# Optimization experiments

Measured on AMD Instinct MI355X. Metric: run time of the kernel, lower is better.

Reference implementation:

```python
import jax, jax.numpy as jnp
import numpy as np

GAMMA = 0.1
ENERGY = 0.5
BATCH = 64
INF = 1e10  # finite 'infinity' so exp(-INF/gamma) underflows to exactly 0


def softdtw_batch(D, gamma):
    """Batched soft-DTW over pairwise frame-distance matrices.
    D: [P, T, T] squared-Euclidean distances. Returns R(T-1,T-1): [P].
    DP is parallelized across anti-diagonals (wavefront)."""
    P, T, _ = D.shape
    iarr = jnp.arange(T)

    def body(carry, k):
        Rm2, Rm1 = carry  # diagonals k-2 and k-1, each [P, T] indexed by row i
        j = k - iarr
        valid = (j >= 0) & (j < T)
        d = D[:, iarr, jnp.clip(j, 0, T - 1)]  # [P, T]
        pad = jnp.full((P, 1), INF, D.dtype)
        r_up = jnp.concatenate([pad, Rm1[:, :-1]], axis=1)      # R(i-1, j)
        r_left = Rm1                                            # R(i, j-1)
        corner = jnp.where(k == 0, jnp.float32(0.0), jnp.float32(INF))
        r_diag = jnp.concatenate([jnp.full((P, 1), 1.0, D.dtype) * corner,
                                  Rm2[:, :-1]], axis=1)         # R(i-1, j-1)
        z = jnp.stack([r_up, r_left, r_diag], axis=0)           # [3, P, T]
        smin = -gamma * jax.nn.logsumexp(-z / gamma, axis=0)
        Rk = jnp.where(valid[None, :], d + smin, INF)
        return (Rm1, Rk), None

    init = (jnp.full((P, T), INF, D.dtype), jnp.full((P, T), INF, D.dtype))
    (_, Rlast), _ = jax.lax.scan(body, init, jnp.arange(2 * T - 1))
    return Rlast[:, T - 1]


def setup_inputs() -> dict:
    key = jax.random.key(0)
    k1, k2 = jax.random.split(key)
    xxx = jax.random.normal(k1, (BATCH, 64, 13), dtype=jnp.float32)
    yyy = jax.random.normal(k2, (BATCH, 64, 13), dtype=jnp.float32)
    return {"xxx": xxx, "yyy": yyy}


def reference(xxx, yyy):
    B = BATCH
    full = jnp.concatenate([xxx, yyy], axis=0)  # [N, T, d]
    N, T, _ = full.shape
    # pairwise squared-Euclidean frame distances: [N, N, T, T]
    sq = jnp.sum(full * full, axis=-1)                      # [N, T]
    dots = jnp.einsum('aid,bjd->abij', full, full)          # [N, N, T, T]
    D = sq[:, None, :, None] + sq[None, :, None, :] - 2.0 * dots
    R = softdtw_batch(D.reshape(N * N, T, T), GAMMA)        # [N*N]
    sim = R.reshape(N, N)
    eye = jnp.eye(N, dtype=bool)
    sim = jnp.where(eye, 0.0, sim)  # i==j pairs skipped in original (left as 0)
    sim = sim / ENERGY
    pos = jnp.diagonal(sim, offset=B)                       # [B]
    positives = jnp.concatenate([pos, pos], axis=0)         # [2B] (source uses +B offset twice)
    loss = jnp.mean(-positives + jax.nn.logsumexp(sim, axis=-1))
    return loss
```

## Files before the change

### kernel.cpp

```cpp
#include <hip/hip_runtime.h>

#define TT 64
#define DIM 13
#define NSEQ 128
#define NPAIRS 8128
#define NWAVE 4064
#define NSTEP (TT + 32 - 1)
#define INFV 1e10f
#define C_EXP 14.4269504088896f
#define C_INV 0.06931471805599453f

typedef _Float16 h2 __attribute__((ext_vector_type(2)));

__device__ __forceinline__ float fdot2(h2 a, h2 b, float c) {
    return __builtin_amdgcn_fdot2(a, b, c, false);
}
__device__ __forceinline__ h2 mkh2(float a, float b) {
    h2 p; p.x = (_Float16)a; p.y = (_Float16)b; return p;
}
__device__ __forceinline__ h2 bch2(unsigned u) { return __builtin_bit_cast(h2, u); }
__device__ __forceinline__ float shr1_inf(float x) {
    int r = __builtin_amdgcn_update_dpp(__builtin_bit_cast(int, INFV),
                                        __builtin_bit_cast(int, x),
                                        0x138, 0xf, 0xf, false);
    return __builtin_bit_cast(float, r);
}
__device__ __forceinline__ float smstep(float S, float lf, float dg, float acc) {
    float m  = fminf(fminf(S, lf), dg);
    float md = __builtin_amdgcn_fmed3f(S, lf, dg);
    float M  = fmaxf(fmaxf(S, lf), dg);
    float s  = 1.0f + __builtin_amdgcn_exp2f(m - md) + __builtin_amdgcn_exp2f(m - M);
    return fmaf(acc, C_EXP, m - __builtin_amdgcn_logf(s));
}

__global__ __launch_bounds__(256) void sdtw_pairs(const float* __restrict__ xxx,
                                                  const float* __restrict__ yyy,
                                                  float* __restrict__ simR) {
    __shared__ unsigned xl[4][7 * 2 * TT];
    const int wave = threadIdx.x >> 6;
    const int lane = threadIdx.x & 63;
    const int half = lane >> 5;
    const int sj   = lane & 31;
    const int p = 2 * (blockIdx.x * 4 + wave) + half;

    int a = (int)((255.0f - sqrtf(65025.0f - 8.0f * (float)p)) * 0.5f);
    if (a < 0) a = 0;
    if (a > 126) a = 126;
    while (a * (255 - a) / 2 > p) a--;
    while ((a + 1) * (254 - a) / 2 <= p) a++;
    const int b = a + 1 + (p - a * (255 - a) / 2);

    h2 yA[7], yB[7];
    float sqyA = 0.f, sqyB = 0.f;
    {
        const float* fb = ((b < 64) ? xxx + (size_t)b * TT * DIM
                                    : yyy + (size_t)(b - 64) * TT * DIM) + (2 * sj) * DIM;
        float vA[DIM], vB[DIM];
#pragma unroll
        for (int c = 0; c < DIM; c++) {
            vA[c] = fb[c];        sqyA += vA[c] * vA[c];
            vB[c] = fb[DIM + c];  sqyB += vB[c] * vB[c];
        }
#pragma unroll
        for (int c = 0; c < 6; c++) {
            yA[c] = mkh2(vA[2 * c], vA[2 * c + 1]);
            yB[c] = mkh2(vB[2 * c], vB[2 * c + 1]);
        }
        yA[6] = mkh2(vA[12], 1.0f);
        yB[6] = mkh2(vB[12], 1.0f);
    }

    {
        const float* fa = (a < 64) ? xxx + (size_t)a * TT * DIM
                                   : yyy + (size_t)(a - 64) * TT * DIM;
        unsigned* xw = xl[wave];
#pragma unroll
        for (int rr = 0; rr < 2; rr++) {
            const int r = sj + 32 * rr;
            const float* fx = fa + r * DIM;
            float xv[DIM], sqx = 0.f;
#pragma unroll
            for (int c = 0; c < DIM; c++) { xv[c] = fx[c]; sqx += xv[c] * xv[c]; }
            unsigned* dst = xw + half * TT + r;
#pragma unroll
            for (int c = 0; c < 6; c++)
                dst[c * 128] = __builtin_bit_cast(unsigned, mkh2(-2.f * xv[2 * c], -2.f * xv[2 * c + 1]));
            dst[6 * 128] = __builtin_bit_cast(unsigned, mkh2(-2.f * xv[12], sqx));
        }
    }
    __syncthreads();

    const unsigned* xp = xl[wave] + half * TT;
    float SA = INFV, SB = INFV;
    float dgA = (sj == 0) ? 0.f : INFV;
    const bool col0 = (sj == 0);
    int ic = (-sj) & (TT - 1);

#pragma unroll 2
    for (int k = 0; k < NSTEP; k++) {
        unsigned w0 = xp[ic];
        unsigned w1 = xp[ic + 1 * 128];
        unsigned w2 = xp[ic + 2 * 128];
        unsigned w3 = xp[ic + 3 * 128];
        unsigned w4 = xp[ic + 4 * 128];
        unsigned w5 = xp[ic + 5 * 128];
        unsigned w6 = xp[ic + 6 * 128];
        ic = (ic + 1) & (TT - 1);

        float aA = sqyA, aB = sqyB;
        aA = fdot2(yA[0], bch2(w0), aA); aB = fdot2(yB[0], bch2(w0), aB);
        aA = fdot2(yA[1], bch2(w1), aA); aB = fdot2(yB[1], bch2(w1), aB);
        aA = fdot2(yA[2], bch2(w2), aA); aB = fdot2(yB[2], bch2(w2), aB);
        aA = fdot2(yA[3], bch2(w3), aA); aB = fdot2(yB[3], bch2(w3), aB);
        aA = fdot2(yA[4], bch2(w4), aA); aB = fdot2(yB[4], bch2(w4), aB);
        aA = fdot2(yA[5], bch2(w5), aA); aB = fdot2(yB[5], bch2(w5), aB);
        aA = fdot2(yA[6], bch2(w6), aA); aB = fdot2(yB[6], bch2(w6), aB);

        float lfA = shr1_inf(SB);
        lfA = col0 ? INFV : lfA;

        float SAold = SA;
        SA = smstep(SA, lfA, dgA, aA);
        SB = smstep(SB, SA, SAold, aB);
        dgA = lfA;
    }

    if (sj == 31) {
        const float r = SB * C_INV;
        simR[a * NSEQ + b] = r;
        simR[b * NSEQ + a] = r;
    }
}

__global__ void row_lse(float* __restrict__ simR) {
    const int r = blockIdx.x;
    const int lane = threadIdx.x;
    const float* rowp = simR + r * NSEQ;
    float v0 = (lane == r) ? 0.f : 2.f * rowp[lane];
    const int c1 = lane + 64;
    float v1 = (c1 == r) ? 0.f : 2.f * rowp[c1];
    float mx = fmaxf(v0, v1);
#pragma unroll
    for (int o = 32; o; o >>= 1) mx = fmaxf(mx, __shfl_xor(mx, o));
    float s = __builtin_amdgcn_exp2f((v0 - mx) * 1.4426950408889634f)
            + __builtin_amdgcn_exp2f((v1 - mx) * 1.4426950408889634f);
#pragma unroll
    for (int o = 32; o; o >>= 1) s += __shfl_xor(s, o);
    if (lane == 0) {
        const int i = r & 63;
        float pos = 2.f * simR[i * NSEQ + i + 64];
        simR[r * NSEQ + r] = mx + 0.6931471805599453f * __builtin_amdgcn_logf(s) - pos;
    }
}

__global__ void final_loss(const float* __restrict__ simR, float* __restrict__ out) {
    __shared__ float red[NSEQ];
    const int tid = threadIdx.x;
    red[tid] = simR[tid * NSEQ + tid];
    __syncthreads();
    if (tid == 0) {
        float tsum = 0.f;
        for (int c = 0; c < NSEQ; c++) tsum += red[c];
        out[0] = tsum / (float)NSEQ;
    }
}

extern "C" void kernel_launch(void* const* d_in, const int* in_sizes, int n_in,
                              void* d_out, int out_size, void* d_ws, size_t ws_size,
                              hipStream_t stream) {
    const float* xxx = (const float*)d_in[0];
    const float* yyy = (const float*)d_in[1];
    float* out = (float*)d_out;
    float* simR = (float*)d_ws;

    sdtw_pairs<<<NWAVE / 4, 256, 0, stream>>>(xxx, yyy, simR);
    row_lse<<<NSEQ, 64, 0, stream>>>(simR);
    final_loss<<<1, NSEQ, 0, stream>>>(simR, out);
}
```

Before: 42.13 us.

## Prefetch LDS row words one step ahead and fuse loss reduction kernels

The wavefront loop now loads the next step's seven packed x-words from LDS before computing the current step, so the LDS reads can overlap the dot-product and soft-min arithmetic. Separately, the per-row logsumexp kernel and the final mean kernel are merged into one 1024-thread block that reduces rows in groups of 8 lanes and sums through shared memory. This removes one kernel launch and a global round-trip. The trade-off is that the fused kernel runs on a single workgroup, and the prefetch slightly raises register pressure.

```diff
diff --git a/kernel.cpp b/kernel.cpp
--- a/kernel.cpp
+++ b/kernel.cpp
@@ -96,25 +96,26 @@
     const bool col0 = (sj == 0);
     int ic = (-sj) & (TT - 1);
 
+    unsigned w[7];
+#pragma unroll
+    for (int c = 0; c < 7; c++) w[c] = xp[ic + c * 128];
+    ic = (ic + 1) & (TT - 1);
+
 #pragma unroll 2
     for (int k = 0; k < NSTEP; k++) {
-        unsigned w0 = xp[ic];
-        unsigned w1 = xp[ic + 1 * 128];
-        unsigned w2 = xp[ic + 2 * 128];
-        unsigned w3 = xp[ic + 3 * 128];
-        unsigned w4 = xp[ic + 4 * 128];
-        unsigned w5 = xp[ic + 5 * 128];
-        unsigned w6 = xp[ic + 6 * 128];
+        unsigned nw[7];
+#pragma unroll
+        for (int c = 0; c < 7; c++) nw[c] = xp[ic + c * 128];
         ic = (ic + 1) & (TT - 1);
 
         float aA = sqyA, aB = sqyB;
-        aA = fdot2(yA[0], bch2(w0), aA); aB = fdot2(yB[0], bch2(w0), aB);
-        aA = fdot2(yA[1], bch2(w1), aA); aB = fdot2(yB[1], bch2(w1), aB);
-        aA = fdot2(yA[2], bch2(w2), aA); aB = fdot2(yB[2], bch2(w2), aB);
-        aA = fdot2(yA[3], bch2(w3), aA); aB = fdot2(yB[3], bch2(w3), aB);
-        aA = fdot2(yA[4], bch2(w4), aA); aB = fdot2(yB[4], bch2(w4), aB);
-        aA = fdot2(yA[5], bch2(w5), aA); aB = fdot2(yB[5], bch2(w5), aB);
-        aA = fdot2(yA[6], bch2(w6), aA); aB = fdot2(yB[6], bch2(w6), aB);
+        aA = fdot2(yA[0], bch2(w[0]), aA); aB = fdot2(yB[0], bch2(w[0]), aB);
+        aA = fdot2(yA[1], bch2(w[1]), aA); aB = fdot2(yB[1], bch2(w[1]), aB);
+        aA = fdot2(yA[2], bch2(w[2]), aA); aB = fdot2(yB[2], bch2(w[2]), aB);
+        aA = fdot2(yA[3], bch2(w[3]), aA); aB = fdot2(yB[3], bch2(w[3]), aB);
+        aA = fdot2(yA[4], bch2(w[4]), aA); aB = fdot2(yB[4], bch2(w[4]), aB);
+        aA = fdot2(yA[5], bch2(w[5]), aA); aB = fdot2(yB[5], bch2(w[5]), aB);
+        aA = fdot2(yA[6], bch2(w[6]), aA); aB = fdot2(yB[6], bch2(w[6]), aB);
 
         float lfA = shr1_inf(SB);
         lfA = col0 ? INFV : lfA;
@@ -123,6 +124,9 @@
         SA = smstep(SA, lfA, dgA, aA);
         SB = smstep(SB, SA, SAold, aB);
         dgA = lfA;
+
+#pragma unroll
+        for (int c = 0; c < 7; c++) w[c] = nw[c];
     }
 
     if (sj == 31) {
@@ -132,36 +136,41 @@
     }
 }
 
-__global__ void row_lse(float* __restrict__ simR) {
-    const int r = blockIdx.x;
-    const int lane = threadIdx.x;
+__global__ __launch_bounds__(1024) void loss_reduce(const float* __restrict__ simR,
+                                                    float* __restrict__ out) {
+    __shared__ float rsum[NSEQ];
+    const int tid = threadIdx.x;
+    const int r  = tid >> 3;
+    const int l8 = tid & 7;
     const float* rowp = simR + r * NSEQ;
-    float v0 = (lane == r) ? 0.f : 2.f * rowp[lane];
-    const int c1 = lane + 64;
-    float v1 = (c1 == r) ? 0.f : 2.f * rowp[c1];
-    float mx = fmaxf(v0, v1);
+
+    float v[16];
 #pragma unroll
-    for (int o = 32; o; o >>= 1) mx = fmaxf(mx, __shfl_xor(mx, o));
-    float s = __builtin_amdgcn_exp2f((v0 - mx) * 1.4426950408889634f)
-            + __builtin_amdgcn_exp2f((v1 - mx) * 1.4426950408889634f);
+    for (int c = 0; c < 16; c++) {
+        const int col = l8 + 8 * c;
+        v[c] = (col == r) ? 0.f : 2.f * rowp[col];
+    }
+    float mx = v[0];
 #pragma unroll
-    for (int o = 32; o; o >>= 1) s += __shfl_xor(s, o);
-    if (lane == 0) {
+    for (int c = 1; c < 16; c++) mx = fmaxf(mx, v[c]);
+#pragma unroll
+    for (int o = 1; o <= 4; o <<= 1) mx = fmaxf(mx, __shfl_xor(mx, o));
+    float s = 0.f;
+#pragma unroll
+    for (int c = 0; c < 16; c++) s += __builtin_amdgcn_exp2f((v[c] - mx) * 1.4426950408889634f);
+#pragma unroll
+    for (int o = 1; o <= 4; o <<= 1) s += __shfl_xor(s, o);
+    if (l8 == 0) {
         const int i = r & 63;
-        float pos = 2.f * simR[i * NSEQ + i + 64];
-        simR[r * NSEQ + r] = mx + 0.6931471805599453f * __builtin_amdgcn_logf(s) - pos;
+        const float pos = 2.f * simR[i * NSEQ + i + 64];
+        rsum[r] = mx + 0.6931471805599453f * __builtin_amdgcn_logf(s) - pos;
     }
-}
-
-__global__ void final_loss(const float* __restrict__ simR, float* __restrict__ out) {
-    __shared__ float red[NSEQ];
-    const int tid = threadIdx.x;
-    red[tid] = simR[tid * NSEQ + tid];
     __syncthreads();
-    if (tid == 0) {
-        float tsum = 0.f;
-        for (int c = 0; c < NSEQ; c++) tsum += red[c];
-        out[0] = tsum / (float)NSEQ;
+    if (tid < 64) {
+        float t = rsum[tid] + rsum[tid + 64];
+#pragma unroll
+        for (int o = 32; o; o >>= 1) t += __shfl_xor(t, o);
+        if (tid == 0) out[0] = t / (float)NSEQ;
     }
 }
 
@@ -174,6 +183,5 @@
     float* simR = (float*)d_ws;
 
     sdtw_pairs<<<NWAVE / 4, 256, 0, stream>>>(xxx, yyy, simR);
-    row_lse<<<NSEQ, 64, 0, stream>>>(simR);
-    final_loss<<<1, NSEQ, 0, stream>>>(simR, out);
+    loss_reduce<<<1, 1024, 0, stream>>>(simR, out);
 }
```

After: 42.97 us. About the same (+2.0%).
